# Kernel tuning notes

Hardware: AMD Instinct MI355X
Metric: run time of the kernel (lower is better)

## Reference

```python
import jax, jax.numpy as jnp
import numpy as np

B, N, D, H = 2, 2048, 1024, 16
DK = D // H


def setup_inputs() -> dict:
    key = jax.random.key(0)
    ks = jax.random.split(key, 12)
    s = D ** -0.5
    inp = {
        "query": jax.random.normal(ks[0], (B, N, D), jnp.float32),
        "key": jax.random.normal(ks[1], (B, N, D), jnp.float32),
        "value": jax.random.normal(ks[2], (B, N, D), jnp.float32),
        # causal mask: 1 = keep, 0 = masked (matches create_causal_mask)
        "mask": jnp.tril(jnp.ones((N, N), jnp.int32)),
        "Wq": jax.random.normal(ks[3], (D, D), jnp.float32) * s,
        "bq": jnp.zeros((D,), jnp.float32),
        "Wk": jax.random.normal(ks[4], (D, D), jnp.float32) * s,
        "bk": jnp.zeros((D,), jnp.float32),
        "Wv": jax.random.normal(ks[5], (D, D), jnp.float32) * s,
        "bv": jnp.zeros((D,), jnp.float32),
        "Wo": jax.random.normal(ks[6], (D, D), jnp.float32) * s,
        "bo": jnp.zeros((D,), jnp.float32),
    }
    return inp


def reference(query, key, value, mask, Wq, bq, Wk, bk, Wv, bv, Wo, bo):
    scale = DK ** -0.5
    # Linear projections (torch nn.Linear: x @ W.T + b), split into heads -> [B,H,N,DK]
    q = (query @ Wq.T + bq).reshape(B, N, H, DK).transpose(0, 2, 1, 3)
    k = (key @ Wk.T + bk).reshape(B, N, H, DK).transpose(0, 2, 1, 3)
    v = (value @ Wv.T + bv).reshape(B, N, H, DK).transpose(0, 2, 1, 3)
    scores = jnp.einsum("bhqd,bhkd->bhqk", q, k) * scale  # [B,H,N,N]
    scores = jnp.where(mask[None, None, :, :] == 0, jnp.float32(-1e9), scores)
    attn = jax.nn.softmax(scores, axis=-1)
    ctx = jnp.einsum("bhqk,bhkd->bhqd", attn, v)  # [B,H,N,DK]
    ctx = ctx.transpose(0, 2, 1, 3).reshape(B, N, D)
    return ctx @ Wo.T + bo
```

## Files before the change

kernel.cpp:

```cpp
#include <hip/hip_runtime.h>
#include <hip/hip_bf16.h>

typedef __attribute__((ext_vector_type(4))) float f32x4;
typedef __attribute__((ext_vector_type(8))) __bf16 bf16x8;
typedef __attribute__((ext_vector_type(8))) unsigned short u16x8;
typedef __attribute__((ext_vector_type(4))) unsigned short u16x4;
typedef __attribute__((ext_vector_type(2))) unsigned int u32x2;
typedef unsigned short u16;

#define DEV static __device__ __forceinline__

DEV u16 f2bf(float f){
  unsigned u = __builtin_bit_cast(unsigned, f);
  u += 0x7fff + ((u >> 16) & 1);
  return (u16)(u >> 16);
}

DEV f32x4 mfma16(bf16x8 a, bf16x8 b, f32x4 c){
  return __builtin_amdgcn_mfma_f32_16x16x32_bf16(a, b, c, 0, 0, 0);
}

DEV void gload16(const void* g, void* l){
  __builtin_amdgcn_global_load_lds((const __attribute__((address_space(1))) void*)g,
                                   (__attribute__((address_space(3))) void*)l,
                                   16, 0, 0);
}

DEV float fexp2(float x){
#if __has_builtin(__builtin_amdgcn_exp2f)
  return __builtin_amdgcn_exp2f(x);
#else
  float r; asm("v_exp_f32 %0, %1" : "=v"(r) : "v"(x)); return r;
#endif
}

__global__ __launch_bounds__(256) void cvt_k(
    const float* __restrict__ s0, const float* __restrict__ s1,
    const float* __restrict__ s2, const float* __restrict__ s3,
    const float* __restrict__ s4, const float* __restrict__ s5,
    const float* __restrict__ s6,
    u16* __restrict__ d0, u16* __restrict__ d1, u16* __restrict__ d2,
    u16* __restrict__ d3, u16* __restrict__ d4, u16* __restrict__ d5,
    u16* __restrict__ d6){
  const int y = blockIdx.y;
  const float* __restrict__ s = y==0?s0:y==1?s1:y==2?s2:y==3?s3:y==4?s4:y==5?s5:s6;
  u16* __restrict__ d         = y==0?d0:y==1?d1:y==2?d2:y==3?d3:y==4?d4:y==5?d5:d6;
  const int n8 = (y < 3) ? (4096*1024/8) : (1024*1024/8);
  for (int i = blockIdx.x*256 + threadIdx.x; i < n8; i += gridDim.x*256){
    f32x4 a = *(const f32x4*)&s[(size_t)i*8];
    f32x4 b = *(const f32x4*)&s[(size_t)i*8 + 4];
    u16x8 h;
    #pragma unroll
    for (int j = 0; j < 4; ++j){ h[j] = f2bf(a[j]); h[j+4] = f2bf(b[j]); }
    *(u16x8*)&d[(size_t)i*8] = h;
  }
}

#define SCL 0.18033688011f
#define THR 11.0f
#define PLD 72

template<int OUT_F32>
__global__ __launch_bounds__(256) void gemm_bt(
    const u16* __restrict__ A0, const u16* __restrict__ A1, const u16* __restrict__ A2,
    const u16* __restrict__ B0, const u16* __restrict__ B1, const u16* __restrict__ B2,
    const float* __restrict__ e0, const float* __restrict__ e1, const float* __restrict__ e2,
    void* __restrict__ C0, void* __restrict__ C1, void* __restrict__ C2){
  __shared__ u16 As[128*32];
  __shared__ u16 Bs[128*32];
  const int z = blockIdx.z;
  const u16* __restrict__ A    = z==0 ? A0 : z==1 ? A1 : A2;
  const u16* __restrict__ Bw   = z==0 ? B0 : z==1 ? B1 : B2;
  const float* __restrict__ bias = z==0 ? e0 : z==1 ? e1 : e2;
  void* __restrict__ Cp        = z==0 ? C0 : z==1 ? C1 : C2;
  const bool vt = (OUT_F32 == 0) && (z == 2);
  const float qs = (OUT_F32 == 0 && z == 0) ? SCL : 1.0f;

  const int tid  = threadIdx.x;
  const int lane = tid & 63, w = tid >> 6;
  const int wr = w >> 1, wc = w & 1;
  const int l16 = lane & 15, lhi = lane >> 4;
  const int bm = vt ? blockIdx.x : blockIdx.y;
  const int bn = vt ? blockIdx.y : blockIdx.x;

  const int srow = w*16 + (lane >> 2);
  const int scol = (lane & 3)*8;
  const u16* Asrc = A  + (size_t)(bm*128 + srow)*1024 + scol;
  const u16* Bsrc = Bw + (size_t)(bn*128 + srow)*1024 + scol;
  u16* Adst0 = As + w*512;
  u16* Bdst0 = Bs + w*512;

  f32x4 acc[4][4] = {};

  for (int k0 = 0; k0 < 1024; k0 += 32){
    __syncthreads();
    gload16(Asrc + k0,             Adst0);
    gload16(Asrc + 64*1024 + k0,   Adst0 + 2048);
    gload16(Bsrc + k0,             Bdst0);
    gload16(Bsrc + 64*1024 + k0,   Bdst0 + 2048);
    __syncthreads();

    bf16x8 af[4], bfr[4];
    #pragma unroll
    for (int mi = 0; mi < 4; ++mi)
      af[mi] = *(const bf16x8*)&As[(wr*64 + mi*16 + l16)*32 + lhi*8];
    #pragma unroll
    for (int nf = 0; nf < 4; ++nf)
      bfr[nf] = *(const bf16x8*)&Bs[(wc*64 + nf*16 + l16)*32 + lhi*8];
    #pragma unroll
    for (int mi = 0; mi < 4; ++mi)
      #pragma unroll
      for (int nf = 0; nf < 4; ++nf)
        acc[mi][nf] = mfma16(af[mi], bfr[nf], acc[mi][nf]);
  }

  #pragma unroll
  for (int mi = 0; mi < 4; ++mi){
    #pragma unroll
    for (int nf = 0; nf < 4; ++nf){
      int row0 = bm*128 + wr*64 + mi*16 + lhi*4;
      int col  = bn*128 + wc*64 + nf*16 + l16;
      float bc = bias[col];
      #pragma unroll
      for (int r = 0; r < 4; ++r){
        int row = row0 + r;
        float val = (acc[mi][nf][r] + (vt ? bias[row] : bc)) * qs;
        if (OUT_F32){
          ((float*)Cp)[(size_t)row*1024 + col] = val;
        } else if (!vt){
          int b = row >> 11, n = row & 2047;
          int h = col >> 6,  dk = col & 63;
          ((u16*)Cp)[(((size_t)(b*16 + h))*2048 + n)*64 + dk] = f2bf(val);
        } else {
          int h = row >> 6,  dk = row & 63;
          int b = col >> 11, n = col & 2047;
          ((u16*)Cp)[(((size_t)(b*16 + h))*64 + dk)*2048 + n] = f2bf(val);
        }
      }
    }
  }
}

__global__ __launch_bounds__(256) void gemm_o64(const u16* __restrict__ A,
                                                const u16* __restrict__ Bw,
                                                const float* __restrict__ bias,
                                                float* __restrict__ C){
  __shared__ u16 As[64*32];
  __shared__ u16 Bs[128*32];
  const int tid  = threadIdx.x;
  const int lane = tid & 63, w = tid >> 6;
  const int wr = w >> 1, wc = w & 1;
  const int l16 = lane & 15, lhi = lane >> 4;
  const int bm = blockIdx.y, bn = blockIdx.x;

  const int srow = w*16 + (lane >> 2);
  const int scol = (lane & 3)*8;
  const u16* Asrc = A  + (size_t)(bm*64  + srow)*1024 + scol;
  const u16* Bsrc = Bw + (size_t)(bn*128 + srow)*1024 + scol;
  u16* Adst0 = As + w*512;
  u16* Bdst0 = Bs + w*512;

  f32x4 acc[2][4] = {};

  for (int k0 = 0; k0 < 1024; k0 += 32){
    __syncthreads();
    gload16(Asrc + k0,             Adst0);
    gload16(Bsrc + k0,             Bdst0);
    gload16(Bsrc + 64*1024 + k0,   Bdst0 + 2048);
    __syncthreads();

    bf16x8 af[2], bfr[4];
    #pragma unroll
    for (int mi = 0; mi < 2; ++mi)
      af[mi] = *(const bf16x8*)&As[(wr*32 + mi*16 + l16)*32 + lhi*8];
    #pragma unroll
    for (int nf = 0; nf < 4; ++nf)
      bfr[nf] = *(const bf16x8*)&Bs[(wc*64 + nf*16 + l16)*32 + lhi*8];
    #pragma unroll
    for (int mi = 0; mi < 2; ++mi)
      #pragma unroll
      for (int nf = 0; nf < 4; ++nf)
        acc[mi][nf] = mfma16(af[mi], bfr[nf], acc[mi][nf]);
  }

  #pragma unroll
  for (int mi = 0; mi < 2; ++mi){
    #pragma unroll
    for (int nf = 0; nf < 4; ++nf){
      int row0 = bm*64 + wr*32 + mi*16 + lhi*4;
      int col  = bn*128 + wc*64 + nf*16 + l16;
      float bv = bias[col];
      #pragma unroll
      for (int r = 0; r < 4; ++r)
        C[(size_t)(row0 + r)*1024 + col] = acc[mi][nf][r] + bv;
    }
  }
}

DEV void sm_tile(int t, int qt, int q_abs,
                 const u16* __restrict__ Ksb, u16* __restrict__ PsW,
                 bf16x8 bq0, bf16x8 bq1,
                 f32x4* ctx, float& m_r, float& l_r,
                 int l16, int lhi, int lane, int swz){
  f32x4 s4[4] = {};
  #pragma unroll
  for (int nf = 0; nf < 4; ++nf){
    bf16x8 ak0 = *(const bf16x8*)&Ksb[(nf*16 + l16)*64 + ((lhi*8) ^ swz)];
    bf16x8 ak1 = *(const bf16x8*)&Ksb[(nf*16 + l16)*64 + ((32 + lhi*8) ^ swz)];
    s4[nf] = mfma16(ak0, bq0, s4[nf]);
    s4[nf] = mfma16(ak1, bq1, s4[nf]);
  }

  if (t == qt){
    #pragma unroll
    for (int nf = 0; nf < 4; ++nf)
      #pragma unroll
      for (int r = 0; r < 4; ++r){
        int kc = t*64 + nf*16 + lhi*4 + r;
        if (kc > q_abs) s4[nf][r] = -1.0e30f;
      }
  }

  float mt = fmaxf(
      fmaxf(fmaxf(fmaxf(s4[0][0],s4[0][1]), fmaxf(s4[0][2],s4[0][3])),
            fmaxf(fmaxf(s4[1][0],s4[1][1]), fmaxf(s4[1][2],s4[1][3]))),
      fmaxf(fmaxf(fmaxf(s4[2][0],s4[2][1]), fmaxf(s4[2][2],s4[2][3])),
            fmaxf(fmaxf(s4[3][0],s4[3][1]), fmaxf(s4[3][2],s4[3][3]))));
  mt = fmaxf(mt, __shfl_xor(mt, 16));
  mt = fmaxf(mt, __shfl_xor(mt, 32));

  if (!__all(mt <= m_r + THR)){
    float mn = fmaxf(m_r, mt);
    float sf = fexp2(m_r - mn);
    m_r = mn;
    l_r *= sf;
    float sfb[4];
    #pragma unroll
    for (int r = 0; r < 4; ++r)
      sfb[r] = __shfl(sf, (lane >> 4)*4 + r);
    #pragma unroll
    for (int dkf = 0; dkf < 4; ++dkf)
      #pragma unroll
      for (int r = 0; r < 4; ++r)
        ctx[dkf][r] *= sfb[r];
  }

  float lt = 0.f;
  u16* prow = PsW + l16*PLD;
  #pragma unroll
  for (int nf = 0; nf < 4; ++nf){
    float p0 = fexp2(s4[nf][0] - m_r);
    float p1 = fexp2(s4[nf][1] - m_r);
    float p2 = fexp2(s4[nf][2] - m_r);
    float p3 = fexp2(s4[nf][3] - m_r);
    lt += (p0 + p1) + (p2 + p3);
    unsigned w0 = __builtin_amdgcn_perm(__builtin_bit_cast(unsigned, p1),
                                        __builtin_bit_cast(unsigned, p0), 0x07060302u);
    unsigned w1 = __builtin_amdgcn_perm(__builtin_bit_cast(unsigned, p3),
                                        __builtin_bit_cast(unsigned, p2), 0x07060302u);
    u32x2 wp = {w0, w1};
    *(u32x2*)&prow[nf*16 + lhi*4] = wp;
  }
  lt += __shfl_xor(lt, 16);
  lt += __shfl_xor(lt, 32);
  l_r += lt;
}

DEV void pv_tile(const u16* __restrict__ Vsb, const u16* __restrict__ PsW,
                 f32x4* ctx, int l16, int lhi, int swz){
  const u16* prow = PsW + l16*PLD;
  __builtin_amdgcn_s_setprio(1);
  #pragma unroll
  for (int ks = 0; ks < 2; ++ks){
    bf16x8 pa = *(const bf16x8*)&prow[ks*32 + lhi*8];
    #pragma unroll
    for (int dkf = 0; dkf < 4; ++dkf){
      bf16x8 vb = *(const bf16x8*)&Vsb[(dkf*16 + l16)*64 + ((ks*32 + lhi*8) ^ swz)];
      ctx[dkf] = mfma16(pa, vb, ctx[dkf]);
    }
  }
  __builtin_amdgcn_s_setprio(0);
}

__global__ __launch_bounds__(256) void attn_k(const u16* __restrict__ Q,
                                              const u16* __restrict__ K,
                                              const u16* __restrict__ Vt,
                                              u16* __restrict__ CTX){
  __shared__ u16 Ks[2][64*64];
  __shared__ u16 Vs[2][64*64];
  __shared__ u16 Ps[4][2][16*PLD];
  const int tid  = threadIdx.x;
  const int lane = tid & 63, w = tid >> 6;
  const int l16 = lane & 15, lhi = lane >> 4;
  const int f  = blockIdx.x;
  const int bh = f & 31;
  const int qt = 31 - (f >> 5);
  const size_t base = (size_t)bh * 2048 * 64;
  const u16* Qb = Q  + base;
  const u16* Kb = K  + base;
  const u16* Vb = Vt + base;
  const int b = bh >> 4, h = bh & 15;

  const int s0 = tid, s1 = tid + 256;
  const int r0 = s0 >> 3, c0 = ((s0 & 7) ^ (r0 & 7))*8;
  const int r1 = s1 >> 3, c1 = ((s1 & 7) ^ (r1 & 7))*8;
  const u16* Ksrc0 = Kb + r0*64 + c0;
  const u16* Ksrc1 = Kb + r1*64 + c1;
  const u16* Vsrc0 = Vb + (size_t)r0*2048 + c0;
  const u16* Vsrc1 = Vb + (size_t)r1*2048 + c1;
  const int swz = (l16 & 7)*8;

  const int q_abs = qt*64 + w*16 + l16;
  bf16x8 bq0 = *(const bf16x8*)&Qb[(size_t)q_abs*64 + lhi*8];
  bf16x8 bq1 = *(const bf16x8*)&Qb[(size_t)q_abs*64 + 32 + lhi*8];

  f32x4 ctx[4] = {};
  float m_r = -3.0e38f, l_r = 0.f;
  u16* Ps0 = &Ps[w][0][0];
  u16* Ps1 = &Ps[w][1][0];

  gload16(Ksrc0, &Ks[0][s0*8]);  gload16(Ksrc1, &Ks[0][s1*8]);
  gload16(Vsrc0, &Vs[0][s0*8]);  gload16(Vsrc1, &Vs[0][s1*8]);
  __syncthreads();

  const int nt = qt + 1;
  for (int t = 0; t < nt; ++t){
    const int pb = t & 1;
    u16* PsC = pb ? Ps1 : Ps0;
    u16* PsP = pb ? Ps0 : Ps1;
    if (t + 1 < nt){
      gload16(Ksrc0 + (t+1)*4096, &Ks[pb^1][s0*8]);
      gload16(Ksrc1 + (t+1)*4096, &Ks[pb^1][s1*8]);
    }
    sm_tile(t, qt, q_abs, Ks[pb], PsC, bq0, bq1, ctx, m_r, l_r, l16, lhi, lane, swz);
    if (t > 0)
      pv_tile(Vs[pb^1], PsP, ctx, l16, lhi, swz);
    __syncthreads();
    if (t + 1 < nt){
      gload16(Vsrc0 + (size_t)(t+1)*64, &Vs[pb^1][s0*8]);
      gload16(Vsrc1 + (size_t)(t+1)*64, &Vs[pb^1][s1*8]);
    }
  }
  pv_tile(Vs[(nt-1)&1], (nt-1)&1 ? Ps1 : Ps0, ctx, l16, lhi, swz);

  float lf[4];
  #pragma unroll
  for (int r = 0; r < 4; ++r)
    lf[r] = __shfl(l_r, (lane >> 4)*4 + r);
  #pragma unroll
  for (int dkf = 0; dkf < 4; ++dkf)
    #pragma unroll
    for (int r = 0; r < 4; ++r){
      int q = qt*64 + w*16 + lhi*4 + r;
      CTX[((size_t)(b*2048 + q))*1024 + h*64 + dkf*16 + l16] = f2bf(ctx[dkf][r] / lf[r]);
    }
}

constexpr int LDP = 40;

__global__ __launch_bounds__(256) void gemm_qkv(
    const float* __restrict__ Aq, const float* __restrict__ Ak, const float* __restrict__ Av,
    const float* __restrict__ Bq, const float* __restrict__ Bk, const float* __restrict__ Bv,
    const float* __restrict__ eq, const float* __restrict__ ek, const float* __restrict__ ev,
    u16* __restrict__ Oq, u16* __restrict__ Ok, u16* __restrict__ Ov){
  __shared__ u16 As[128][LDP];
  __shared__ u16 Bs[128][LDP];
  const int z = blockIdx.z;
  const float* __restrict__ A   = z == 0 ? Aq : z == 1 ? Ak : Av;
  const float* __restrict__ W   = z == 0 ? Bq : z == 1 ? Bk : Bv;
  const float* __restrict__ bias= z == 0 ? eq : z == 1 ? ek : ev;
  u16* __restrict__ C           = z == 0 ? Oq : z == 1 ? Ok : Ov;
  const bool vt = (z == 2);
  const float qs = (z == 0) ? SCL : 1.0f;

  const int tid  = threadIdx.x;
  const int lane = tid & 63, wv = tid >> 6;
  const int wr = wv >> 1, wc = wv & 1;
  const int l16 = lane & 15, lhi = lane >> 4;
  const int bm = vt ? blockIdx.x : blockIdx.y;
  const int bn = vt ? blockIdx.y : blockIdx.x;
  const int K = 1024;

  f32x4 acc[4][4] = {};

  for (int k0 = 0; k0 < K; k0 += 32){
    __syncthreads();
    #pragma unroll
    for (int j = 0; j < 4; ++j){
      int s = tid + j*256;
      int row = s >> 3, c4 = s & 7;
      f32x4 v = *(const f32x4*)&A[(size_t)(bm*128 + row)*K + k0 + c4*4];
      u16x4 hh;
      #pragma unroll
      for (int i = 0; i < 4; ++i) hh[i] = f2bf(v[i]);
      *(u16x4*)&As[row][c4*4] = hh;
    }
    #pragma unroll
    for (int j = 0; j < 4; ++j){
      int s = tid + j*256;
      int row = s >> 3, c4 = s & 7;
      f32x4 v = *(const f32x4*)&W[(size_t)(bn*128 + row)*K + k0 + c4*4];
      u16x4 hh;
      #pragma unroll
      for (int i = 0; i < 4; ++i) hh[i] = f2bf(v[i]);
      *(u16x4*)&Bs[row][c4*4] = hh;
    }
    __syncthreads();

    bf16x8 af[4], bfr[4];
    #pragma unroll
    for (int mi = 0; mi < 4; ++mi)
      af[mi] = *(const bf16x8*)&As[wr*64 + mi*16 + l16][lhi*8];
    #pragma unroll
    for (int nf = 0; nf < 4; ++nf)
      bfr[nf] = *(const bf16x8*)&Bs[wc*64 + nf*16 + l16][lhi*8];
    #pragma unroll
    for (int mi = 0; mi < 4; ++mi)
      #pragma unroll
      for (int nf = 0; nf < 4; ++nf)
        acc[mi][nf] = mfma16(af[mi], bfr[nf], acc[mi][nf]);
  }

  #pragma unroll
  for (int mi = 0; mi < 4; ++mi){
    #pragma unroll
    for (int nf = 0; nf < 4; ++nf){
      int row0 = bm*128 + wr*64 + mi*16 + lhi*4;
      int col  = bn*128 + wc*64 + nf*16 + l16;
      float bc = bias[col];
      #pragma unroll
      for (int r = 0; r < 4; ++r){
        int row = row0 + r;
        float val = (acc[mi][nf][r] + (vt ? bias[row] : bc)) * qs;
        if (!vt){
          int b = row >> 11, n = row & 2047;
          int h = col >> 6,  dk = col & 63;
          C[(((size_t)(b*16 + h))*2048 + n)*64 + dk] = f2bf(val);
        } else {
          int h = row >> 6,  dk = row & 63;
          int b = col >> 11, n = col & 2047;
          C[(((size_t)(b*16 + h))*64 + dk)*2048 + n] = f2bf(val);
        }
      }
    }
  }
}

extern "C" void kernel_launch(void* const* d_in, const int* in_sizes, int n_in,
                              void* d_out, int out_size, void* d_ws, size_t ws_size,
                              hipStream_t stream){
  const float* q  = (const float*)d_in[0];
  const float* k  = (const float*)d_in[1];
  const float* v  = (const float*)d_in[2];
  const float* Wq = (const float*)d_in[4];  const float* bq = (const float*)d_in[5];
  const float* Wk = (const float*)d_in[6];  const float* bk = (const float*)d_in[7];
  const float* Wv = (const float*)d_in[8];  const float* bv = (const float*)d_in[9];
  const float* Wo = (const float*)d_in[10]; const float* bo = (const float*)d_in[11];
  float* out = (float*)d_out;
  dim3 blk(256);

  const size_t need = (size_t)(3*4194304 + 4*1048576 + 3*4194304) * 2;
  if (ws_size >= need){
    u16* Xqb = (u16*)d_ws;
    u16* Xkb = Xqb + 4194304;
    u16* Xvb = Xkb + 4194304;
    u16* Wqb = Xvb + 4194304;
    u16* Wkb = Wqb + 1048576;
    u16* Wvb = Wkb + 1048576;
    u16* Wob = Wvb + 1048576;
    u16* Qw  = Wob + 1048576;
    u16* Kw  = Qw + 4194304;
    u16* Vw  = Kw + 4194304;
    u16* Cw  = Xqb;

    cvt_k<<<dim3(512, 7), blk, 0, stream>>>(q, k, v, Wq, Wk, Wv, Wo,
                                            Xqb, Xkb, Xvb, Wqb, Wkb, Wvb, Wob);
    gemm_bt<0><<<dim3(8, 32, 3), blk, 0, stream>>>(
        Xqb, Xkb, Wvb, Wqb, Wkb, Xvb, bq, bk, bv,
        (void*)Qw, (void*)Kw, (void*)Vw);
    attn_k<<<dim3(1024), blk, 0, stream>>>(Qw, Kw, Vw, Cw);
    gemm_o64<<<dim3(8, 64), blk, 0, stream>>>(Cw, Wob, bo, out);
  } else {
    u16* Qw = (u16*)d_ws;
    u16* Kw = Qw + (size_t)4096*1024;
    u16* Vw = Kw + (size_t)4096*1024;
    u16* Cw = Vw + (size_t)4096*1024;
    gemm_qkv<<<dim3(8, 32, 3), blk, 0, stream>>>(q, k, Wv, Wq, Wk, v, bq, bk, bv,
                                                 Qw, Kw, Vw);
    attn_k<<<dim3(1024), blk, 0, stream>>>(Qw, Kw, Vw, Cw);
    gemm_o64<<<dim3(8, 64), blk, 0, stream>>>(Cw, (const u16*)Wo, bo, out);
  }
}
```

Before: 122.3 us.

## Fuse activation fp32-to-bf16 conversion into QKV GEMM and remap block order

Activations are no longer converted to bf16 in a separate pass; the QKV projection kernel now loads fp32 X tiles straight into LDS with async global-to-LDS loads, using an XOR-swizzled layout, and packs them to bf16 in registers with v_cvt_pk_bf16_f32 while reading fragments. Only the weights are still pre-converted. The K step grows to 64, and both GEMMs switch to a 1D grid with a remapped block order meant to group blocks for L2 locality. This removes a full read and write of the activations, at the cost of 48KB of LDS per block (which may lower occupancy) and extra conversion work inside the GEMM inner loop.

New measurement: 135.3 us. +10.6%, slower.

```diff
diff --git a/kernel.cpp b/kernel.cpp
--- a/kernel.cpp
+++ b/kernel.cpp
@@ -16,6 +16,12 @@
   return (u16)(u >> 16);
 }
 
+DEV unsigned cvtpk(float lo, float hi){
+  unsigned r;
+  asm("v_cvt_pk_bf16_f32 %0, %1, %2" : "=v"(r) : "v"(lo), "v"(hi));
+  return r;
+}
+
 DEV f32x4 mfma16(bf16x8 a, bf16x8 b, f32x4 c){
   return __builtin_amdgcn_mfma_f32_16x16x32_bf16(a, b, c, 0, 0, 0);
 }
@@ -34,84 +40,110 @@
 #endif
 }
 
-__global__ __launch_bounds__(256) void cvt_k(
-    const float* __restrict__ s0, const float* __restrict__ s1,
-    const float* __restrict__ s2, const float* __restrict__ s3,
-    const float* __restrict__ s4, const float* __restrict__ s5,
-    const float* __restrict__ s6,
-    u16* __restrict__ d0, u16* __restrict__ d1, u16* __restrict__ d2,
-    u16* __restrict__ d3, u16* __restrict__ d4, u16* __restrict__ d5,
-    u16* __restrict__ d6){
-  const int y = blockIdx.y;
-  const float* __restrict__ s = y==0?s0:y==1?s1:y==2?s2:y==3?s3:y==4?s4:y==5?s5:s6;
-  u16* __restrict__ d         = y==0?d0:y==1?d1:y==2?d2:y==3?d3:y==4?d4:y==5?d5:d6;
-  const int n8 = (y < 3) ? (4096*1024/8) : (1024*1024/8);
-  for (int i = blockIdx.x*256 + threadIdx.x; i < n8; i += gridDim.x*256){
-    f32x4 a = *(const f32x4*)&s[(size_t)i*8];
-    f32x4 b = *(const f32x4*)&s[(size_t)i*8 + 4];
-    u16x8 h;
-    #pragma unroll
-    for (int j = 0; j < 4; ++j){ h[j] = f2bf(a[j]); h[j+4] = f2bf(b[j]); }
-    *(u16x8*)&d[(size_t)i*8] = h;
-  }
-}
-
 #define SCL 0.18033688011f
 #define THR 11.0f
 #define PLD 72
 
-template<int OUT_F32>
-__global__ __launch_bounds__(256) void gemm_bt(
-    const u16* __restrict__ A0, const u16* __restrict__ A1, const u16* __restrict__ A2,
-    const u16* __restrict__ B0, const u16* __restrict__ B1, const u16* __restrict__ B2,
-    const float* __restrict__ e0, const float* __restrict__ e1, const float* __restrict__ e2,
-    void* __restrict__ C0, void* __restrict__ C1, void* __restrict__ C2){
-  __shared__ u16 As[128*32];
-  __shared__ u16 Bs[128*32];
-  const int z = blockIdx.z;
-  const u16* __restrict__ A    = z==0 ? A0 : z==1 ? A1 : A2;
-  const u16* __restrict__ Bw   = z==0 ? B0 : z==1 ? B1 : B2;
-  const float* __restrict__ bias = z==0 ? e0 : z==1 ? e1 : e2;
-  void* __restrict__ Cp        = z==0 ? C0 : z==1 ? C1 : C2;
-  const bool vt = (OUT_F32 == 0) && (z == 2);
-  const float qs = (OUT_F32 == 0 && z == 0) ? SCL : 1.0f;
-
-  const int tid  = threadIdx.x;
-  const int lane = tid & 63, w = tid >> 6;
+__global__ __launch_bounds__(256) void cvtW_k(
+    const float* __restrict__ s0, const float* __restrict__ s1,
+    const float* __restrict__ s2, const float* __restrict__ s3,
+    u16* __restrict__ d0, u16* __restrict__ d1,
+    u16* __restrict__ d2, u16* __restrict__ d3){
+  const int y = blockIdx.y;
+  const float* __restrict__ s = y==0?s0:y==1?s1:y==2?s2:s3;
+  u16* __restrict__ d         = y==0?d0:y==1?d1:y==2?d2:d3;
+  const int i = blockIdx.x*256 + threadIdx.x;
+  f32x4 a = *(const f32x4*)&s[(size_t)i*8];
+  f32x4 b = *(const f32x4*)&s[(size_t)i*8 + 4];
+  u16x8 h;
+  #pragma unroll
+  for (int j = 0; j < 4; ++j){ h[j] = f2bf(a[j]); h[j+4] = f2bf(b[j]); }
+  *(u16x8*)&d[(size_t)i*8] = h;
+}
+
+DEV bf16x8 rdH(const u16* Hs, int r, int kc, int lhi, int l7){
+  int gr = (kc*4 + lhi) ^ l7;
+  return *(const bf16x8*)&Hs[r*64 + gr*8];
+}
+
+DEV bf16x8 rdF(const float* Fs, int r, int kc, int lhi, int l15){
+  int g0 = kc*8 + lhi*2, g1 = g0 + 1;
+  f32x4 a = *(const f32x4*)&Fs[r*64 + ((g0 ^ l15)*4)];
+  f32x4 b = *(const f32x4*)&Fs[r*64 + ((g1 ^ l15)*4)];
+  union { unsigned u[4]; bf16x8 v; } x;
+  x.u[0] = cvtpk(a[0], a[1]);
+  x.u[1] = cvtpk(a[2], a[3]);
+  x.u[2] = cvtpk(b[0], b[1]);
+  x.u[3] = cvtpk(b[2], b[3]);
+  return x.v;
+}
+
+__global__ __launch_bounds__(256) void gemm_qkv2(
+    const float* __restrict__ Xq, const float* __restrict__ Xk, const float* __restrict__ Xv,
+    const u16* __restrict__ Wq, const u16* __restrict__ Wk, const u16* __restrict__ Wv,
+    const float* __restrict__ Bq, const float* __restrict__ Bk, const float* __restrict__ Bv,
+    u16* __restrict__ Oq, u16* __restrict__ Ok, u16* __restrict__ Ov){
+  __shared__ float Fs[128*64];
+  __shared__ u16  Hs[128*64];
+
+  const int f = blockIdx.x;
+  const int xc = f & 7, g = f >> 3;
+  const int p  = xc*12 + (g >> 3);
+  const int bn8 = g & 7;
+  const int z = p >> 5, bm32 = p & 31;
+  const bool vt = (z == 2);
+  const int bm = vt ? bn8 : bm32;
+  const int bn = vt ? bm32 : bn8;
+
+  const float* __restrict__ Xz = z==0 ? Xq : z==1 ? Xk : Xv;
+  const u16*  __restrict__ Wz  = z==0 ? Wq : z==1 ? Wk : Wv;
+  const float* __restrict__ bias = z==0 ? Bq : z==1 ? Bk : Bv;
+  u16* __restrict__ C = z==0 ? Oq : z==1 ? Ok : Ov;
+  const float qs = (z==0) ? SCL : 1.0f;
+
+  const int tid = threadIdx.x, lane = tid & 63, w = tid >> 6;
   const int wr = w >> 1, wc = w & 1;
-  const int l16 = lane & 15, lhi = lane >> 4;
-  const int bm = vt ? blockIdx.x : blockIdx.y;
-  const int bn = vt ? blockIdx.y : blockIdx.x;
-
-  const int srow = w*16 + (lane >> 2);
-  const int scol = (lane & 3)*8;
-  const u16* Asrc = A  + (size_t)(bm*128 + srow)*1024 + scol;
-  const u16* Bsrc = Bw + (size_t)(bn*128 + srow)*1024 + scol;
-  u16* Adst0 = As + w*512;
-  u16* Bdst0 = Bs + w*512;
+  const int l16 = lane & 15, lhi = lane >> 4, l7 = l16 & 7;
+
+  const int frow = tid >> 4, fcol = ((tid & 15) ^ (frow & 15)) * 4;
+  const int hrow = tid >> 3, hcol = ((tid & 7) ^ (hrow & 7)) * 8;
+  const int fblk = vt ? bn : bm;
+  const int hblk = vt ? bm : bn;
+  const float* Fsrc = Xz + (size_t)(fblk*128 + frow)*1024 + fcol;
+  const u16*  Hsrc  = Wz + (size_t)(hblk*128 + hrow)*1024 + hcol;
 
   f32x4 acc[4][4] = {};
 
-  for (int k0 = 0; k0 < 1024; k0 += 32){
+  for (int k0 = 0; k0 < 1024; k0 += 64){
     __syncthreads();
-    gload16(Asrc + k0,             Adst0);
-    gload16(Asrc + 64*1024 + k0,   Adst0 + 2048);
-    gload16(Bsrc + k0,             Bdst0);
-    gload16(Bsrc + 64*1024 + k0,   Bdst0 + 2048);
+    #pragma unroll
+    for (int j = 0; j < 8; ++j)
+      gload16(Fsrc + k0 + (size_t)j*16*1024, Fs + j*1024 + w*256);
+    #pragma unroll
+    for (int j = 0; j < 4; ++j)
+      gload16(Hsrc + k0 + (size_t)j*32*1024, Hs + j*2048 + w*512);
     __syncthreads();
 
-    bf16x8 af[4], bfr[4];
-    #pragma unroll
-    for (int mi = 0; mi < 4; ++mi)
-      af[mi] = *(const bf16x8*)&As[(wr*64 + mi*16 + l16)*32 + lhi*8];
-    #pragma unroll
-    for (int nf = 0; nf < 4; ++nf)
-      bfr[nf] = *(const bf16x8*)&Bs[(wc*64 + nf*16 + l16)*32 + lhi*8];
-    #pragma unroll
-    for (int mi = 0; mi < 4; ++mi)
-      #pragma unroll
-      for (int nf = 0; nf < 4; ++nf)
-        acc[mi][nf] = mfma16(af[mi], bfr[nf], acc[mi][nf]);
+    #pragma unroll
+    for (int kc = 0; kc < 2; ++kc){
+      bf16x8 fa[4], fb[4];
+      if (!vt){
+        #pragma unroll
+        for (int mi = 0; mi < 4; ++mi) fa[mi] = rdF(Fs, wr*64 + mi*16 + l16, kc, lhi, l16);
+        #pragma unroll
+        for (int nf = 0; nf < 4; ++nf) fb[nf] = rdH(Hs, wc*64 + nf*16 + l16, kc, lhi, l7);
+      } else {
+        #pragma unroll
+        for (int mi = 0; mi < 4; ++mi) fa[mi] = rdH(Hs, wr*64 + mi*16 + l16, kc, lhi, l7);
+        #pragma unroll
+        for (int nf = 0; nf < 4; ++nf) fb[nf] = rdF(Fs, wc*64 + nf*16 + l16, kc, lhi, l16);
+      }
+      #pragma unroll
+      for (int mi = 0; mi < 4; ++mi)
+        #pragma unroll
+        for (int nf = 0; nf < 4; ++nf)
+          acc[mi][nf] = mfma16(fa[mi], fb[nf], acc[mi][nf]);
+    }
   }
 
   #pragma unroll
@@ -125,16 +157,14 @@
       for (int r = 0; r < 4; ++r){
         int row = row0 + r;
         float val = (acc[mi][nf][r] + (vt ? bias[row] : bc)) * qs;
-        if (OUT_F32){
-          ((float*)Cp)[(size_t)row*1024 + col] = val;
-        } else if (!vt){
+        if (!vt){
           int b = row >> 11, n = row & 2047;
           int h = col >> 6,  dk = col & 63;
-          ((u16*)Cp)[(((size_t)(b*16 + h))*2048 + n)*64 + dk] = f2bf(val);
+          C[(((size_t)(b*16 + h))*2048 + n)*64 + dk] = f2bf(val);
         } else {
           int h = row >> 6,  dk = row & 63;
           int b = col >> 11, n = col & 2047;
-          ((u16*)Cp)[(((size_t)(b*16 + h))*64 + dk)*2048 + n] = f2bf(val);
+          C[(((size_t)(b*16 + h))*64 + dk)*2048 + n] = f2bf(val);
         }
       }
     }
@@ -147,11 +177,13 @@
                                                 float* __restrict__ C){
   __shared__ u16 As[64*32];
   __shared__ u16 Bs[128*32];
+  const int f = blockIdx.x;
+  const int bm = (f & 7)*8 + ((f >> 3) >> 3);
+  const int bn = (f >> 3) & 7;
   const int tid  = threadIdx.x;
   const int lane = tid & 63, w = tid >> 6;
   const int wr = w >> 1, wc = w & 1;
   const int l16 = lane & 15, lhi = lane >> 4;
-  const int bm = blockIdx.y, bn = blockIdx.x;
 
   const int srow = w*16 + (lane >> 2);
   const int scol = (lane & 3)*8;
@@ -356,96 +388,6 @@
     }
 }
 
-constexpr int LDP = 40;
-
-__global__ __launch_bounds__(256) void gemm_qkv(
-    const float* __restrict__ Aq, const float* __restrict__ Ak, const float* __restrict__ Av,
-    const float* __restrict__ Bq, const float* __restrict__ Bk, const float* __restrict__ Bv,
-    const float* __restrict__ eq, const float* __restrict__ ek, const float* __restrict__ ev,
-    u16* __restrict__ Oq, u16* __restrict__ Ok, u16* __restrict__ Ov){
-  __shared__ u16 As[128][LDP];
-  __shared__ u16 Bs[128][LDP];
-  const int z = blockIdx.z;
-  const float* __restrict__ A   = z == 0 ? Aq : z == 1 ? Ak : Av;
-  const float* __restrict__ W   = z == 0 ? Bq : z == 1 ? Bk : Bv;
-  const float* __restrict__ bias= z == 0 ? eq : z == 1 ? ek : ev;
-  u16* __restrict__ C           = z == 0 ? Oq : z == 1 ? Ok : Ov;
-  const bool vt = (z == 2);
-  const float qs = (z == 0) ? SCL : 1.0f;
-
-  const int tid  = threadIdx.x;
-  const int lane = tid & 63, wv = tid >> 6;
-  const int wr = wv >> 1, wc = wv & 1;
-  const int l16 = lane & 15, lhi = lane >> 4;
-  const int bm = vt ? blockIdx.x : blockIdx.y;
-  const int bn = vt ? blockIdx.y : blockIdx.x;
-  const int K = 1024;
-
-  f32x4 acc[4][4] = {};
-
-  for (int k0 = 0; k0 < K; k0 += 32){
-    __syncthreads();
-    #pragma unroll
-    for (int j = 0; j < 4; ++j){
-      int s = tid + j*256;
-      int row = s >> 3, c4 = s & 7;
-      f32x4 v = *(const f32x4*)&A[(size_t)(bm*128 + row)*K + k0 + c4*4];
-      u16x4 hh;
-      #pragma unroll
-      for (int i = 0; i < 4; ++i) hh[i] = f2bf(v[i]);
-      *(u16x4*)&As[row][c4*4] = hh;
-    }
-    #pragma unroll
-    for (int j = 0; j < 4; ++j){
-      int s = tid + j*256;
-      int row = s >> 3, c4 = s & 7;
-      f32x4 v = *(const f32x4*)&W[(size_t)(bn*128 + row)*K + k0 + c4*4];
-      u16x4 hh;
-      #pragma unroll
-      for (int i = 0; i < 4; ++i) hh[i] = f2bf(v[i]);
-      *(u16x4*)&Bs[row][c4*4] = hh;
-    }
-    __syncthreads();
-
-    bf16x8 af[4], bfr[4];
-    #pragma unroll
-    for (int mi = 0; mi < 4; ++mi)
-      af[mi] = *(const bf16x8*)&As[wr*64 + mi*16 + l16][lhi*8];
-    #pragma unroll
-    for (int nf = 0; nf < 4; ++nf)
-      bfr[nf] = *(const bf16x8*)&Bs[wc*64 + nf*16 + l16][lhi*8];
-    #pragma unroll
-    for (int mi = 0; mi < 4; ++mi)
-      #pragma unroll
-      for (int nf = 0; nf < 4; ++nf)
-        acc[mi][nf] = mfma16(af[mi], bfr[nf], acc[mi][nf]);
-  }
-
-  #pragma unroll
-  for (int mi = 0; mi < 4; ++mi){
-    #pragma unroll
-    for (int nf = 0; nf < 4; ++nf){
-      int row0 = bm*128 + wr*64 + mi*16 + lhi*4;
-      int col  = bn*128 + wc*64 + nf*16 + l16;
-      float bc = bias[col];
-      #pragma unroll
-      for (int r = 0; r < 4; ++r){
-        int row = row0 + r;
-        float val = (acc[mi][nf][r] + (vt ? bias[row] : bc)) * qs;
-        if (!vt){
-          int b = row >> 11, n = row & 2047;
-          int h = col >> 6,  dk = col & 63;
-          C[(((size_t)(b*16 + h))*2048 + n)*64 + dk] = f2bf(val);
-        } else {
-          int h = row >> 6,  dk = row & 63;
-          int b = col >> 11, n = col & 2047;
-          C[(((size_t)(b*16 + h))*64 + dk)*2048 + n] = f2bf(val);
-        }
-      }
-    }
-  }
-}
-
 extern "C" void kernel_launch(void* const* d_in, const int* in_sizes, int n_in,
                               void* d_out, int out_size, void* d_ws, size_t ws_size,
                               hipStream_t stream){
@@ -459,35 +401,18 @@
   float* out = (float*)d_out;
   dim3 blk(256);
 
-  const size_t need = (size_t)(3*4194304 + 4*1048576 + 3*4194304) * 2;
-  if (ws_size >= need){
-    u16* Xqb = (u16*)d_ws;
-    u16* Xkb = Xqb + 4194304;
-    u16* Xvb = Xkb + 4194304;
-    u16* Wqb = Xvb + 4194304;
-    u16* Wkb = Wqb + 1048576;
-    u16* Wvb = Wkb + 1048576;
-    u16* Wob = Wvb + 1048576;
-    u16* Qw  = Wob + 1048576;
-    u16* Kw  = Qw + 4194304;
-    u16* Vw  = Kw + 4194304;
-    u16* Cw  = Xqb;
-
-    cvt_k<<<dim3(512, 7), blk, 0, stream>>>(q, k, v, Wq, Wk, Wv, Wo,
-                                            Xqb, Xkb, Xvb, Wqb, Wkb, Wvb, Wob);
-    gemm_bt<0><<<dim3(8, 32, 3), blk, 0, stream>>>(
-        Xqb, Xkb, Wvb, Wqb, Wkb, Xvb, bq, bk, bv,
-        (void*)Qw, (void*)Kw, (void*)Vw);
-    attn_k<<<dim3(1024), blk, 0, stream>>>(Qw, Kw, Vw, Cw);
-    gemm_o64<<<dim3(8, 64), blk, 0, stream>>>(Cw, Wob, bo, out);
-  } else {
-    u16* Qw = (u16*)d_ws;
-    u16* Kw = Qw + (size_t)4096*1024;
-    u16* Vw = Kw + (size_t)4096*1024;
-    u16* Cw = Vw + (size_t)4096*1024;
-    gemm_qkv<<<dim3(8, 32, 3), blk, 0, stream>>>(q, k, Wv, Wq, Wk, v, bq, bk, bv,
-                                                 Qw, Kw, Vw);
-    attn_k<<<dim3(1024), blk, 0, stream>>>(Qw, Kw, Vw, Cw);
-    gemm_o64<<<dim3(8, 64), blk, 0, stream>>>(Cw, (const u16*)Wo, bo, out);
-  }
-}
+  u16* Wqb = (u16*)d_ws;
+  u16* Wkb = Wqb + 1048576;
+  u16* Wvb = Wkb + 1048576;
+  u16* Wob = Wvb + 1048576;
+  u16* Qw  = Wob + 1048576;
+  u16* Kw  = Qw + 4194304;
+  u16* Vw  = Kw + 4194304;
+  u16* Cw  = Vw + 4194304;
+
+  cvtW_k<<<dim3(512, 4), blk, 0, stream>>>(Wq, Wk, Wv, Wo, Wqb, Wkb, Wvb, Wob);
+  gemm_qkv2<<<dim3(768), blk, 0, stream>>>(q, k, v, Wqb, Wkb, Wvb,
+                                           bq, bk, bv, Qw, Kw, Vw);
+  attn_k<<<dim3(1024), blk, 0, stream>>>(Qw, Kw, Vw, Cw);
+  gemm_o64<<<dim3(512), blk, 0, stream>>>(Cw, Wob, bo, out);
+}
```
